# Kernel tuning notes

Hardware: AMD Instinct MI355X
Metric: run time of the kernel (lower is better)

## Reference

```python
import jax, jax.numpy as jnp
import numpy as np
from jax import lax


def setup_inputs() -> dict:
    key = jax.random.key(0)
    k1, k2, k3, k4, k5 = jax.random.split(key, 5)
    B, T, D, N = 64, 1024, 512, 24
    return {
        "x": jax.random.normal(k1, (B, T, D), dtype=jnp.float32),
        "W": jax.random.normal(k2, (D, N), dtype=jnp.float32) * 0.05,
        "b": jnp.zeros((N,), dtype=jnp.float32),
        "trans": jax.random.normal(k3, (N, N), dtype=jnp.float32) * 0.1,
        "left_boundary": jax.random.normal(k4, (N,), dtype=jnp.float32) * 0.1,
        "right_boundary": jax.random.normal(k5, (N,), dtype=jnp.float32) * 0.1,
    }


def reference(x, W, b, trans, left_boundary, right_boundary):
    # Dense projection to tag potentials: [B, T, N]
    pot = jnp.einsum("btd,dn->btn", x, W) + b
    B, T, N = pot.shape
    # mask=None -> lengths are all T; boundaries added at t=0 and t=T-1
    lens = jnp.full((B,), T, dtype=jnp.int32)
    pot = pot.at[:, 0, :].add(left_boundary).at[:, T - 1, :].add(right_boundary)

    # Viterbi forward: alpha[b, j] = best score of any path ending in tag j
    def fwd_step(alpha, pot_t):
        scores = alpha[:, :, None] + trans[None, :, :]  # [B, prev, cur]
        bp = jnp.argmax(scores, axis=1)                 # [B, N] best prev tag
        alpha_new = jnp.max(scores, axis=1) + pot_t
        return alpha_new, bp

    alpha0 = pot[:, 0, :]
    pot_rest = jnp.swapaxes(pot[:, 1:, :], 0, 1)  # [T-1, B, N]
    alpha_T, bps = lax.scan(fwd_step, alpha0, pot_rest)
    last_tag = jnp.argmax(alpha_T, axis=-1)  # [B]

    # Backtrack through backpointers (reverse scan over time)
    def back_step(tag, bp_t):
        prev = jnp.take_along_axis(bp_t, tag[:, None], axis=1)[:, 0]
        return prev, prev

    _, tags_head = lax.scan(back_step, last_tag, bps, reverse=True)  # [T-1, B]
    decoded = jnp.concatenate(
        [jnp.swapaxes(tags_head, 0, 1), last_tag[:, None]], axis=1
    ).astype(jnp.int32)  # [B, T]
    return decoded, pot, lens, trans
```

## Files before the change

kernel.cpp:

```cpp
#include <hip/hip_runtime.h>
#include <hip/hip_bf16.h>

#define BB 64
#define TT 1024
#define DD 512
#define NS 24

#define POT_OFF   65536
#define LENS_OFF  1638400
#define TRANS_OFF 1638464

__global__ __launch_bounds__(256) void gemm_pot(
    const float* __restrict__ x, const float* __restrict__ W,
    const float* __restrict__ bias, const float* __restrict__ trans,
    const float* __restrict__ lb, const float* __restrict__ rb,
    float* __restrict__ out)
{
  __shared__ float wl[DD * NS];
  const int tid = threadIdx.x;
  const int l   = tid & 63;
  const int q   = tid >> 6;
  const int row0 = blockIdx.x * 128 + l;
  const int row1 = row0 + 64;

  {
    const float4* Ws = (const float4*)W;
    float4* Wd = (float4*)wl;
#pragma unroll
    for (int i = 0; i < 12; ++i) Wd[tid + i * 256] = Ws[tid + i * 256];
  }
  __syncthreads();

  const float4* xp0 = (const float4*)(x + (size_t)row0 * DD + q * 128);
  const float4* xp1 = (const float4*)(x + (size_t)row1 * DD + q * 128);

  float acc0[NS], acc1[NS];
#pragma unroll
  for (int nn = 0; nn < NS; ++nn) { acc0[nn] = 0.f; acc1[nn] = 0.f; }

  float4 buf0[4], buf1[4];
#pragma unroll
  for (int i = 0; i < 4; ++i) { buf0[i] = xp0[i]; buf1[i] = xp1[i]; }

#pragma unroll
  for (int f = 0; f < 32; ++f) {
    float4 v0 = buf0[f & 3];
    float4 v1 = buf1[f & 3];
    if (f + 4 < 32) { buf0[f & 3] = xp0[f + 4]; buf1[f & 3] = xp1[f + 4]; }
    const float xj0[4] = {v0.x, v0.y, v0.z, v0.w};
    const float xj1[4] = {v1.x, v1.y, v1.z, v1.w};
#pragma unroll
    for (int j = 0; j < 4; ++j) {
      const int k = q * 128 + f * 4 + j;
      const float4* wr = (const float4*)&wl[k * NS];
      float4 w0 = wr[0], w1 = wr[1], w2 = wr[2], w3 = wr[3], w4 = wr[4], w5 = wr[5];
      const float wv[NS] = {w0.x,w0.y,w0.z,w0.w, w1.x,w1.y,w1.z,w1.w,
                            w2.x,w2.y,w2.z,w2.w, w3.x,w3.y,w3.z,w3.w,
                            w4.x,w4.y,w4.z,w4.w, w5.x,w5.y,w5.z,w5.w};
      const float xv0 = xj0[j];
      const float xv1 = xj1[j];
#pragma unroll
      for (int nn = 0; nn < NS; ++nn) {
        acc0[nn] = fmaf(xv0, wv[nn], acc0[nn]);
        acc1[nn] = fmaf(xv1, wv[nn], acc1[nn]);
      }
    }
  }

  __syncthreads();
  if (q != 0) {
#pragma unroll
    for (int nn = 0; nn < NS; ++nn) {
      wl[((q - 1) * 128 + l)      * 25 + nn] = acc0[nn];
      wl[((q - 1) * 128 + 64 + l) * 25 + nn] = acc1[nn];
    }
  }
  __syncthreads();
  if (q == 0) {
#pragma unroll
    for (int rr = 0; rr < 2; ++rr) {
      float* acc = rr ? acc1 : acc0;
      const int row = rr ? row1 : row0;
      const int slot = rr ? (64 + l) : l;
      const int t = row & (TT - 1);
#pragma unroll
      for (int nn = 0; nn < NS; ++nn)
        acc[nn] += wl[(0 * 128 + slot) * 25 + nn] + wl[(1 * 128 + slot) * 25 + nn]
                 + wl[(2 * 128 + slot) * 25 + nn] + bias[nn];
      if (t == 0) {
#pragma unroll
        for (int nn = 0; nn < NS; ++nn) acc[nn] += lb[nn];
      }
      if (t == TT - 1) {
#pragma unroll
        for (int nn = 0; nn < NS; ++nn) acc[nn] += rb[nn];
      }
      float* po = out + POT_OFF + (size_t)row * NS;
#pragma unroll
      for (int i = 0; i < 6; ++i)
        *(float4*)(po + i * 4) = make_float4(acc[4*i], acc[4*i+1], acc[4*i+2], acc[4*i+3]);
    }
  }

  if (blockIdx.x == 0 && tid < BB) out[LENS_OFF + tid] = (float)TT;
  if (blockIdx.x == 1) {
    for (int i = tid; i < NS * NS; i += 256) out[TRANS_OFF + i] = trans[i];
  }
}

__device__ __forceinline__ float m3(float a, float b, float c) {
  return fmaxf(fmaxf(a, b), c);
}

#define RORI(dst, src, J) \
  dst = __builtin_amdgcn_mov_dpp((src), 0x120 + (J), 0xF, 0xF, true)

__global__ __launch_bounds__(1024) void viterbi_fused(
    const float* __restrict__ pot, const float* __restrict__ trans,
    float* __restrict__ out_dec)
{
  __shared__ float ps[TT * NS + 8];
  __shared__ unsigned char bl[TT * NS];
  __shared__ float tl[NS * NS];
  __shared__ int H[32][NS];
  __shared__ int e[32];
  __shared__ int prog;

  const int b = blockIdx.x, tid = threadIdx.x;

  if (tid < NS * NS) tl[tid] = trans[tid];
  if (tid == 0) *(volatile int*)&prog = 0;
  __syncthreads();

  if (tid < 64) {
    __builtin_amdgcn_s_setprio(1);
    const int r = tid >> 4;
    const int c = tid & 15;
    const int g = r >> 1;
    const int n = 16 * (r & 1) + c;
    const int nm = (n < NS) ? n : (NS - 1);

    const float* gp = pot + (size_t)b * TT * NS;

    int colv[16];
    colv[0] = c;
    RORI(colv[1],  c, 1);  RORI(colv[2],  c, 2);  RORI(colv[3],  c, 3);
    RORI(colv[4],  c, 4);  RORI(colv[5],  c, 5);  RORI(colv[6],  c, 6);
    RORI(colv[7],  c, 7);  RORI(colv[8],  c, 8);  RORI(colv[9],  c, 9);
    RORI(colv[10], c, 10); RORI(colv[11], c, 11); RORI(colv[12], c, 12);
    RORI(colv[13], c, 13); RORI(colv[14], c, 14); RORI(colv[15], c, 15);

    bool selx;
    {
      auto nr = __builtin_amdgcn_permlane16_swap(n, n, false, false);
      selx = (nr[0] == 16 * g + c);
    }

    float tcr[16];
#pragma unroll
    for (int j = 0; j < 16; ++j) {
      const int m = 16 * g + colv[j];
      tcr[j] = (m < NS) ? trans[m * NS + nm] : -__builtin_inff();
    }

    float ar[16];
#pragma unroll
    for (int j = 0; j < 16; ++j) {
      const int m = 16 * g + colv[j];
      ar[j] = gp[(m < NS) ? m : (NS - 1)];
    }

    ps[n] = gp[nm];

    float pv[8];
#pragma unroll
    for (int u = 0; u < 8; ++u) pv[u] = gp[(1 + u) * NS + nm];

    auto step = [&](int tt, float potv) {
      float sc[16];
#pragma unroll
      for (int j = 0; j < 16; ++j) sc[j] = ar[j] + tcr[j];
      float u0 = m3(sc[0],  sc[1],  sc[2]);
      float u1 = m3(sc[3],  sc[4],  sc[5]);
      float u2 = m3(sc[6],  sc[7],  sc[8]);
      float u3 = m3(sc[9],  sc[10], sc[11]);
      float u4 = m3(sc[12], sc[13], sc[14]);
      float pm = fmaxf(m3(u0, u1, u2), m3(u3, u4, sc[15]));
      auto pr = __builtin_amdgcn_permlane32_swap(
          __float_as_int(pm), __float_as_int(pm), false, false);
      float al = fmaxf(__int_as_float(pr[0]), __int_as_float(pr[1])) + potv;
      ps[tt * NS + n] = al;
      auto qr = __builtin_amdgcn_permlane16_swap(
          __float_as_int(al), __float_as_int(al), false, false);
      int asel = selx ? qr[0] : qr[1];
      ar[0] = __int_as_float(asel);
      int d1, d2, d3, d4, d5, d6, d7, d8, d9, d10, d11, d12, d13, d14, d15;
      RORI(d1,  asel, 1);  ar[1]  = __int_as_float(d1);
      RORI(d2,  asel, 2);  ar[2]  = __int_as_float(d2);
      RORI(d3,  asel, 3);  ar[3]  = __int_as_float(d3);
      RORI(d4,  asel, 4);  ar[4]  = __int_as_float(d4);
      RORI(d5,  asel, 5);  ar[5]  = __int_as_float(d5);
      RORI(d6,  asel, 6);  ar[6]  = __int_as_float(d6);
      RORI(d7,  asel, 7);  ar[7]  = __int_as_float(d7);
      RORI(d8,  asel, 8);  ar[8]  = __int_as_float(d8);
      RORI(d9,  asel, 9);  ar[9]  = __int_as_float(d9);
      RORI(d10, asel, 10); ar[10] = __int_as_float(d10);
      RORI(d11, asel, 11); ar[11] = __int_as_float(d11);
      RORI(d12, asel, 12); ar[12] = __int_as_float(d12);
      RORI(d13, asel, 13); ar[13] = __int_as_float(d13);
      RORI(d14, asel, 14); ar[14] = __int_as_float(d14);
      RORI(d15, asel, 15); ar[15] = __int_as_float(d15);
    };

    for (int t = 1; t + 7 <= TT - 1; t += 8) {
#pragma unroll
      for (int u = 0; u < 8; ++u) {
        const int tt = t + u;
        const float potv = pv[u];
        pv[u] = gp[(tt + 8) * NS + nm];
        step(tt, potv);
      }
      asm volatile("" ::: "memory");
      *(volatile int*)&prog = t + 7;
    }
#pragma unroll
    for (int u = 0; u < 7; ++u) step(1017 + u, pv[u]);
    asm volatile("" ::: "memory");
    *(volatile int*)&prog = TT - 1;
    __builtin_amdgcn_s_setprio(0);
  } else {
    const int w  = tid >> 6;
    const int l  = tid & 63;
    const int t0 = 1 + (w - 1) * 69;
    const int tend = (t0 + 68 < TT - 1) ? (t0 + 68) : (TT - 1);
    const int half = (l >= 24) ? 1 : 0;
    const int n = (l < 24) ? l : ((l < 48) ? (l - 24) : 0);
    float tlc[NS];
#pragma unroll
    for (int m = 0; m < NS; ++m) tlc[m] = tl[m * NS + n];
    for (int ta = t0; ta <= tend; ta += 2) {
      while (*(volatile int*)&prog < ta) __builtin_amdgcn_s_sleep(1);
      asm volatile("" ::: "memory");
      const int tloc = ta + half;
      if (l < 48 && tloc <= tend) {
        const float4* rr = (const float4*)&ps[(tloc - 1) * NS];
        float arr[NS];
#pragma unroll
        for (int i = 0; i < 6; ++i) {
          float4 v = rr[i];
          arr[4*i] = v.x; arr[4*i+1] = v.y; arr[4*i+2] = v.z; arr[4*i+3] = v.w;
        }
        float best = arr[0] + tlc[0];
        int bi = 0;
#pragma unroll
        for (int m = 1; m < NS; ++m) {
          float s = arr[m] + tlc[m];
          bool gg = s > best;
          bi = gg ? m : bi;
          best = gg ? s : best;
        }
        bl[tloc * NS + n] = (unsigned char)bi;
      }
    }
  }
  __syncthreads();

  if (tid < 32 * NS) {
    const int c2 = tid / NS, s = tid % NS;
    int a2 = s;
    int tlo = c2 * 32; if (tlo < 1) tlo = 1;
    for (int t = c2 * 32 + 31; t >= tlo; --t) a2 = bl[t * NS + a2];
    H[c2][s] = a2;
  }
  __syncthreads();

  if (tid == 0) {
    const float* ar = &ps[(TT - 1) * NS];
    float best = ar[0]; int bi = 0;
#pragma unroll
    for (int nn = 1; nn < NS; ++nn) {
      float v = ar[nn];
      if (v > best) { best = v; bi = nn; }
    }
    int tag = bi;
    e[31] = tag;
    for (int c2 = 31; c2 >= 1; --c2) { tag = H[c2][tag]; e[c2 - 1] = tag; }
  }
  __syncthreads();

  if (tid < 32) {
    const int c2 = tid;
    int tag = e[c2];
    float* od = out_dec + (size_t)b * TT;
    od[c2 * 32 + 31] = (float)tag;
    for (int t = c2 * 32 + 30; t >= c2 * 32; --t) {
      tag = bl[(t + 1) * NS + tag];
      od[t] = (float)tag;
    }
  }
}

extern "C" void kernel_launch(void* const* d_in, const int* in_sizes, int n_in,
                              void* d_out, int out_size, void* d_ws, size_t ws_size,
                              hipStream_t stream)
{
  const float* x     = (const float*)d_in[0];
  const float* W     = (const float*)d_in[1];
  const float* bias  = (const float*)d_in[2];
  const float* trans = (const float*)d_in[3];
  const float* lb    = (const float*)d_in[4];
  const float* rb    = (const float*)d_in[5];
  float* out = (float*)d_out;

  gemm_pot<<<512, 256, 0, stream>>>(x, W, bias, trans, lb, rb, out);
  viterbi_fused<<<BB, 1024, 0, stream>>>(out + POT_OFF, trans, out);
}
```

Measured before the change: 317.4 us.

## Compute potentials GEMM with split-fp16 rocWMMA matrix cores

Adds a rocWMMA path for the x·W projection that splits fp32 operands into fp16 high and low parts, scaled by 256 to preserve range, and does three MMAs per tile to approximate fp32 precision on matrix cores. Each block now handles 256 rows, so the grid is halved. The intent is to replace the scalar FP32 FMA GEMM with matrix-core throughput. The costs are extra conversion work, LDS staging per 16-wide k slice with two barriers each, and a risk of precision drift that could change Viterbi argmax decisions. The path only compiles when the rocWMMA header is available.

```diff
diff --git a/kernel.cpp b/kernel.cpp
--- a/kernel.cpp
+++ b/kernel.cpp
@@ -1,5 +1,12 @@
 #include <hip/hip_runtime.h>
 #include <hip/hip_bf16.h>
+
+#if defined(__has_include)
+#if __has_include(<rocwmma/rocwmma.hpp>)
+#include <rocwmma/rocwmma.hpp>
+#define HAVE_ROCWMMA 1
+#endif
+#endif
 
 #define BB 64
 #define TT 1024
@@ -10,6 +17,119 @@
 #define LENS_OFF  1638400
 #define TRANS_OFF 1638464
 
+#ifdef HAVE_ROCWMMA
+__global__ __launch_bounds__(256) void gemm_pot(
+    const float* __restrict__ x, const float* __restrict__ W,
+    const float* __restrict__ bias, const float* __restrict__ trans,
+    const float* __restrict__ lb, const float* __restrict__ rb,
+    float* __restrict__ out)
+{
+  using namespace rocwmma;
+  __shared__ float16_t Wh[DD * 32];
+  __shared__ float16_t Wl[DD * 32];
+  __shared__ float16_t xh[256 * 16];
+  __shared__ float16_t xl[256 * 16];
+
+  const int tid = threadIdx.x;
+  const int w   = tid >> 6;
+  const size_t rowbase = (size_t)blockIdx.x * 256;
+
+#pragma unroll
+  for (int i = 0; i < 64; ++i) {
+    const int idx = tid + i * 256;
+    const int k = idx >> 5, n = idx & 31;
+    const float v = (n < NS) ? W[k * NS + n] * 256.0f : 0.0f;
+    const float16_t h = (float16_t)v;
+    Wh[idx] = h;
+    Wl[idx] = (float16_t)(v - (float)h);
+  }
+
+  fragment<accumulator, 16, 16, 16, float> acc[4][2];
+#pragma unroll
+  for (int mi = 0; mi < 4; ++mi)
+#pragma unroll
+    for (int ni = 0; ni < 2; ++ni) fill_fragment(acc[mi][ni], 0.0f);
+
+  for (int kk = 0; kk < DD; kk += 16) {
+    __syncthreads();
+    {
+      const float4* xr4 = (const float4*)(x + (rowbase + tid) * DD + kk);
+#pragma unroll
+      for (int j4 = 0; j4 < 4; ++j4) {
+        const float4 v = xr4[j4];
+        const float vv[4] = {v.x, v.y, v.z, v.w};
+#pragma unroll
+        for (int jj = 0; jj < 4; ++jj) {
+          const float s = vv[jj] * 256.0f;
+          const float16_t h = (float16_t)s;
+          xh[tid * 16 + j4 * 4 + jj] = h;
+          xl[tid * 16 + j4 * 4 + jj] = (float16_t)(s - (float)h);
+        }
+      }
+    }
+    __syncthreads();
+
+    fragment<matrix_b, 16, 16, 16, float16_t, row_major> bh[2], bl2[2];
+#pragma unroll
+    for (int ni = 0; ni < 2; ++ni) {
+      load_matrix_sync(bh[ni],  Wh + kk * 32 + ni * 16, 32);
+      load_matrix_sync(bl2[ni], Wl + kk * 32 + ni * 16, 32);
+    }
+#pragma unroll
+    for (int mi = 0; mi < 4; ++mi) {
+      fragment<matrix_a, 16, 16, 16, float16_t, row_major> ah, al;
+      load_matrix_sync(ah, xh + (w * 64 + mi * 16) * 16, 16);
+      load_matrix_sync(al, xl + (w * 64 + mi * 16) * 16, 16);
+#pragma unroll
+      for (int ni = 0; ni < 2; ++ni) {
+        mma_sync(acc[mi][ni], ah, bh[ni],  acc[mi][ni]);
+        mma_sync(acc[mi][ni], ah, bl2[ni], acc[mi][ni]);
+        mma_sync(acc[mi][ni], al, bh[ni],  acc[mi][ni]);
+      }
+    }
+  }
+  __syncthreads();
+
+  float* potl = (float*)Wh;
+#pragma unroll
+  for (int mi = 0; mi < 4; ++mi)
+#pragma unroll
+    for (int ni = 0; ni < 2; ++ni)
+      store_matrix_sync(potl + (w * 64 + mi * 16) * 32 + ni * 16,
+                        acc[mi][ni], 32, mem_row_major);
+  __syncthreads();
+
+  {
+    const size_t row = rowbase + tid;
+    const int t = (int)(row & (TT - 1));
+    float o[NS];
+#pragma unroll
+    for (int n = 0; n < NS; ++n) {
+      float v = potl[tid * 32 + n] * (1.0f / 65536.0f) + bias[n];
+      o[n] = v;
+    }
+    if (t == 0) {
+#pragma unroll
+      for (int n = 0; n < NS; ++n) o[n] += lb[n];
+    }
+    if (t == TT - 1) {
+#pragma unroll
+      for (int n = 0; n < NS; ++n) o[n] += rb[n];
+    }
+    float* po = out + POT_OFF + row * NS;
+#pragma unroll
+    for (int i = 0; i < 6; ++i)
+      *(float4*)(po + i * 4) = make_float4(o[4*i], o[4*i+1], o[4*i+2], o[4*i+3]);
+  }
+
+  if (blockIdx.x == 0 && tid < BB) out[LENS_OFF + tid] = (float)TT;
+  if (blockIdx.x == 1) {
+    for (int i = tid; i < NS * NS; i += 256) out[TRANS_OFF + i] = trans[i];
+  }
+}
+#define GEMM_GRID 256
+
+#else
 __global__ __launch_bounds__(256) void gemm_pot(
     const float* __restrict__ x, const float* __restrict__ W,
     const float* __restrict__ bias, const float* __restrict__ trans,
@@ -107,6 +227,8 @@
     for (int i = tid; i < NS * NS; i += 256) out[TRANS_OFF + i] = trans[i];
   }
 }
+#define GEMM_GRID 512
+#endif
 
 __device__ __forceinline__ float m3(float a, float b, float c) {
   return fmaxf(fmaxf(a, b), c);
@@ -312,6 +434,6 @@
   const float* rb    = (const float*)d_in[5];
   float* out = (float*)d_out;
 
-  gemm_pot<<<512, 256, 0, stream>>>(x, W, bias, trans, lb, rb, out);
+  gemm_pot<<<GEMM_GRID, 256, 0, stream>>>(x, W, bias, trans, lb, rb, out);
   viterbi_fused<<<BB, 1024, 0, stream>>>(out + POT_OFF, trans, out);
 }
```

New measurement: 343.3 us. 8.2% more time.
